# Kernel tuning notes

Hardware: AMD Instinct MI355X
Metric: run time of the kernel (lower is better)

## Reference

```python
import jax, jax.numpy as jnp
import numpy as np

N = 50000   # nodes
E = 800000  # edges (avg degree 16)
D = 96      # input feature dim
U = 96      # units (== D, so no dense_i projection)


def _glorot(key, fan_in, fan_out):
    limit = np.sqrt(6.0 / (fan_in + fan_out)).astype(np.float32)
    return jax.random.uniform(key, (fan_in, fan_out), jnp.float32, -limit, limit)


def setup_inputs() -> dict:
    key = jax.random.key(0)
    ks = jax.random.split(key, 8)
    X = jax.random.normal(ks[0], (N, D), jnp.float32)
    row = jax.random.randint(ks[1], (E,), 0, N, jnp.int32)   # destination nodes
    col = jax.random.randint(ks[2], (E,), 0, N, jnp.int32)   # source nodes
    a_vals = jax.random.uniform(ks[3], (E,), jnp.float32)    # adjacency values
    return {
        "X": X,
        "a_vals": a_vals,
        "Wn": _glorot(ks[4], D, U), "bn": jnp.zeros((U,), jnp.float32),
        "Wgi": _glorot(ks[5], D, U), "bgi": jnp.zeros((U,), jnp.float32),
        "Wgn": _glorot(ks[6], U, U), "bgn": jnp.zeros((U,), jnp.float32),
        "row": row, "col": col,
    }


def reference(X, a_vals, Wn, bn, Wgi, bgi, Wgn, bgn, row, col):
    # new_X = dense_n(X); new_X = A @ new_X  (SpMM via gather + segment_sum)
    newX = X @ Wn + bn                       # [N, U]
    msgs = a_vals[:, None] * newX[col]       # [E, U]
    agg = jax.ops.segment_sum(msgs, row, num_segments=N)  # [N, U]
    # gate = sigmoid(dense_gate_i(X) + dense_gate_n(agg))
    gate = jax.nn.sigmoid(X @ Wgi + bgi + agg @ Wgn + bgn)
    # units == inp_dim -> no dense_i; gated residual combine
    return agg * gate + X * (1.0 - gate)
```

## Files before the change

kernel.cpp:

```cpp
#include <hip/hip_runtime.h>
#include <math.h>


#define DU 96
#define DU4 24
#define CAP 64

typedef unsigned int uint;
typedef unsigned short ushort;
typedef __attribute__((ext_vector_type(8))) short short8;
typedef __attribute__((ext_vector_type(4))) float f32x4;

__device__ inline uint bf16r(float x) {
  uint u = __float_as_uint(x);
  return (u + 0x7FFFu + ((u >> 16) & 1u)) >> 16;
}

__global__ __launch_bounds__(256) void k_fuse1(
    const float* __restrict__ X, const float* __restrict__ Wn,
    const float* __restrict__ bn, const float* __restrict__ Wgi,
    const float* __restrict__ Wgn, const int* __restrict__ row,
    const int* __restrict__ col, const float* __restrict__ a_vals,
    ushort* __restrict__ Xb, ushort* __restrict__ newXb,
    ushort* __restrict__ WTgi, ushort* __restrict__ WTgn,
    int* __restrict__ cnt, int2* __restrict__ epad, int N, int E, int ntile) {
  __shared__ ushort WL[9216];
  __shared__ ushort Xs[64][104];
  const int tid = threadIdx.x;
  const int lane = tid & 63, w = tid >> 6;
  const int m = lane & 15, q = lane >> 4;

  if ((int)blockIdx.x < ntile) {
    if (blockIdx.x == 0) {
      for (int i = tid; i < DU * DU; i += 256) {
        int n = i / DU, k = i % DU;
        WTgi[i] = (ushort)bf16r(Wgi[k * DU + n]);
      }
    } else if (blockIdx.x == 1) {
      for (int i = tid; i < DU * DU; i += 256) {
        int n = i / DU, k = i % DU;
        WTgn[i] = (ushort)bf16r(Wgn[k * DU + n]);
      }
    }
    for (int idx = tid; idx < 9216; idx += 256) {
      int j = idx & 7, ln = (idx >> 3) & 63, tk = idx >> 9;
      int ks = tk / 6, t = tk % 6;
      int k = ks * 32 + (ln >> 4) * 8 + j;
      int n = t * 16 + (ln & 15);
      WL[idx] = (ushort)bf16r(Wn[k * DU + n]);
    }
    const int row0 = blockIdx.x * 64;
    for (int i = tid; i < 64 * 48; i += 256) {
      int r = i / 48, cu = i % 48;
      int gr = row0 + r;
      uint packed = 0;
      if (gr < N) {
        float2 v = ((const float2*)X)[(size_t)gr * 48 + cu];
        packed = bf16r(v.x) | (bf16r(v.y) << 16);
        ((uint*)Xb)[(size_t)gr * 48 + cu] = packed;
      }
      *(uint*)&Xs[r][cu * 2] = packed;
    }
    __syncthreads();

    f32x4 acc[6];
#pragma unroll
    for (int t = 0; t < 6; ++t) acc[t] = (f32x4){0.f, 0.f, 0.f, 0.f};
#pragma unroll
    for (int ks = 0; ks < 3; ++ks) {
      short8 af = *(const short8*)&Xs[w * 16 + m][ks * 32 + q * 8];
#pragma unroll
      for (int t = 0; t < 6; ++t) {
        short8 bf = *(const short8*)&WL[((ks * 6 + t) * 64 + lane) * 8];
        acc[t] = __builtin_amdgcn_mfma_f32_16x16x32_bf16(af, bf, acc[t], 0, 0, 0);
      }
    }
    __syncthreads();
#pragma unroll
    for (int t = 0; t < 6; ++t) {
      int c = t * 16 + m;
      float bb = bn[c];
#pragma unroll
      for (int i = 0; i < 4; ++i)
        Xs[w * 16 + q * 4 + i][c] = (ushort)bf16r(acc[t][i] + bb);
    }
    __syncthreads();
    for (int i = tid; i < 64 * 48; i += 256) {
      int r = i / 48, cu = i % 48;
      int gr = row0 + r;
      if (gr < N) ((uint*)newXb)[(size_t)gr * 48 + cu] = *(uint*)&Xs[r][cu * 2];
    }
  }

  {
    const int g = blockIdx.x & 7;
    const int sub = blockIdx.x >> 3;
    const int nsub = gridDim.x >> 3;
    const int d0 = (int)((long long)N * g >> 3);
    const int d1 = (int)((long long)N * (g + 1) >> 3);
    for (int i = sub * 256 + tid; i < E; i += nsub * 256) {
      int d = row[i];
      if (d >= d0 && d < d1) {
        int slot = atomicAdd(&cnt[d], 1);
        epad[(size_t)d * CAP + slot] = make_int2(col[i], __float_as_int(a_vals[i]));
      }
    }
  }
}

__global__ __launch_bounds__(256) void k_agg(const ushort* __restrict__ newXb,
                                             const int* __restrict__ cnt,
                                             const int2* __restrict__ epad,
                                             ushort* __restrict__ aggb, int N) {
  int i = blockIdx.x * 256 + threadIdx.x;
  int r = i / 12;
  int c = i % 12;
  if (r >= N) return;
  int e1 = cnt[r];
  if (e1 > CAP) e1 = CAP;
  const int2* ep = epad + (size_t)r * CAP;
  float accA[8], accB[8];
#pragma unroll
  for (int k = 0; k < 8; ++k) { accA[k] = 0.f; accB[k] = 0.f; }
  int e = 0;
  for (; e + 4 <= e1; e += 4) {
    int2 p0 = ep[e + 0];
    int2 p1 = ep[e + 1];
    int2 p2 = ep[e + 2];
    int2 p3 = ep[e + 3];
    uint4 v0 = *(const uint4*)(newXb + (size_t)p0.x * DU + c * 8);
    uint4 v1 = *(const uint4*)(newXb + (size_t)p1.x * DU + c * 8);
    uint4 v2 = *(const uint4*)(newXb + (size_t)p2.x * DU + c * 8);
    uint4 v3 = *(const uint4*)(newXb + (size_t)p3.x * DU + c * 8);
    float a0 = __int_as_float(p0.y), a1 = __int_as_float(p1.y);
    float a2 = __int_as_float(p2.y), a3 = __int_as_float(p3.y);
    accA[0] = fmaf(a0, __uint_as_float(v0.x << 16), accA[0]);
    accA[1] = fmaf(a0, __uint_as_float(v0.x & 0xFFFF0000u), accA[1]);
    accA[2] = fmaf(a0, __uint_as_float(v0.y << 16), accA[2]);
    accA[3] = fmaf(a0, __uint_as_float(v0.y & 0xFFFF0000u), accA[3]);
    accA[4] = fmaf(a0, __uint_as_float(v0.z << 16), accA[4]);
    accA[5] = fmaf(a0, __uint_as_float(v0.z & 0xFFFF0000u), accA[5]);
    accA[6] = fmaf(a0, __uint_as_float(v0.w << 16), accA[6]);
    accA[7] = fmaf(a0, __uint_as_float(v0.w & 0xFFFF0000u), accA[7]);
    accB[0] = fmaf(a1, __uint_as_float(v1.x << 16), accB[0]);
    accB[1] = fmaf(a1, __uint_as_float(v1.x & 0xFFFF0000u), accB[1]);
    accB[2] = fmaf(a1, __uint_as_float(v1.y << 16), accB[2]);
    accB[3] = fmaf(a1, __uint_as_float(v1.y & 0xFFFF0000u), accB[3]);
    accB[4] = fmaf(a1, __uint_as_float(v1.z << 16), accB[4]);
    accB[5] = fmaf(a1, __uint_as_float(v1.z & 0xFFFF0000u), accB[5]);
    accB[6] = fmaf(a1, __uint_as_float(v1.w << 16), accB[6]);
    accB[7] = fmaf(a1, __uint_as_float(v1.w & 0xFFFF0000u), accB[7]);
    accA[0] = fmaf(a2, __uint_as_float(v2.x << 16), accA[0]);
    accA[1] = fmaf(a2, __uint_as_float(v2.x & 0xFFFF0000u), accA[1]);
    accA[2] = fmaf(a2, __uint_as_float(v2.y << 16), accA[2]);
    accA[3] = fmaf(a2, __uint_as_float(v2.y & 0xFFFF0000u), accA[3]);
    accA[4] = fmaf(a2, __uint_as_float(v2.z << 16), accA[4]);
    accA[5] = fmaf(a2, __uint_as_float(v2.z & 0xFFFF0000u), accA[5]);
    accA[6] = fmaf(a2, __uint_as_float(v2.w << 16), accA[6]);
    accA[7] = fmaf(a2, __uint_as_float(v2.w & 0xFFFF0000u), accA[7]);
    accB[0] = fmaf(a3, __uint_as_float(v3.x << 16), accB[0]);
    accB[1] = fmaf(a3, __uint_as_float(v3.x & 0xFFFF0000u), accB[1]);
    accB[2] = fmaf(a3, __uint_as_float(v3.y << 16), accB[2]);
    accB[3] = fmaf(a3, __uint_as_float(v3.y & 0xFFFF0000u), accB[3]);
    accB[4] = fmaf(a3, __uint_as_float(v3.z << 16), accB[4]);
    accB[5] = fmaf(a3, __uint_as_float(v3.z & 0xFFFF0000u), accB[5]);
    accB[6] = fmaf(a3, __uint_as_float(v3.w << 16), accB[6]);
    accB[7] = fmaf(a3, __uint_as_float(v3.w & 0xFFFF0000u), accB[7]);
  }
  for (; e < e1; ++e) {
    int2 p = ep[e];
    uint4 v = *(const uint4*)(newXb + (size_t)p.x * DU + c * 8);
    float a = __int_as_float(p.y);
    accA[0] = fmaf(a, __uint_as_float(v.x << 16), accA[0]);
    accA[1] = fmaf(a, __uint_as_float(v.x & 0xFFFF0000u), accA[1]);
    accA[2] = fmaf(a, __uint_as_float(v.y << 16), accA[2]);
    accA[3] = fmaf(a, __uint_as_float(v.y & 0xFFFF0000u), accA[3]);
    accA[4] = fmaf(a, __uint_as_float(v.z << 16), accA[4]);
    accA[5] = fmaf(a, __uint_as_float(v.z & 0xFFFF0000u), accA[5]);
    accA[6] = fmaf(a, __uint_as_float(v.w << 16), accA[6]);
    accA[7] = fmaf(a, __uint_as_float(v.w & 0xFFFF0000u), accA[7]);
  }
#pragma unroll
  for (int k = 0; k < 8; ++k) accA[k] += accB[k];
  uint4 o;
  o.x = bf16r(accA[0]) | (bf16r(accA[1]) << 16);
  o.y = bf16r(accA[2]) | (bf16r(accA[3]) << 16);
  o.z = bf16r(accA[4]) | (bf16r(accA[5]) << 16);
  o.w = bf16r(accA[6]) | (bf16r(accA[7]) << 16);
  *(uint4*)(aggb + (size_t)r * DU + c * 8) = o;
}

__global__ __launch_bounds__(256) void k_gateM(const ushort* __restrict__ Xb,
                                               const ushort* __restrict__ aggb,
                                               const ushort* __restrict__ WTgi,
                                               const ushort* __restrict__ WTgn,
                                               const float* __restrict__ bgi,
                                               const float* __restrict__ bgn,
                                               const float* __restrict__ X,
                                               float* __restrict__ Out, int N) {
  __shared__ float Gs[64][100];
  const int tid = threadIdx.x;
  const int lane = tid & 63, w = tid >> 6;
  const int m = lane & 15, q = lane >> 4;
  const int row0 = blockIdx.x * 64;
  int ar = row0 + w * 16 + m;
  if (ar > N - 1) ar = N - 1;

  f32x4 acc[6];
#pragma unroll
  for (int t = 0; t < 6; ++t) acc[t] = (f32x4){0.f, 0.f, 0.f, 0.f};

#pragma unroll
  for (int ks = 0; ks < 3; ++ks) {
    short8 af = *(const short8*)(Xb + (size_t)ar * DU + ks * 32 + q * 8);
#pragma unroll
    for (int t = 0; t < 6; ++t) {
      short8 bf = *(const short8*)(WTgi + (size_t)(t * 16 + m) * DU + ks * 32 + q * 8);
      acc[t] = __builtin_amdgcn_mfma_f32_16x16x32_bf16(af, bf, acc[t], 0, 0, 0);
    }
  }
#pragma unroll
  for (int ks = 0; ks < 3; ++ks) {
    short8 af = *(const short8*)(aggb + (size_t)ar * DU + ks * 32 + q * 8);
#pragma unroll
    for (int t = 0; t < 6; ++t) {
      short8 bf = *(const short8*)(WTgn + (size_t)(t * 16 + m) * DU + ks * 32 + q * 8);
      acc[t] = __builtin_amdgcn_mfma_f32_16x16x32_bf16(af, bf, acc[t], 0, 0, 0);
    }
  }

#pragma unroll
  for (int t = 0; t < 6; ++t) {
    int c = t * 16 + m;
    float bb = bgi[c] + bgn[c];
#pragma unroll
    for (int i = 0; i < 4; ++i) {
      float z = acc[t][i] + bb;
      Gs[w * 16 + q * 4 + i][c] = 1.f / (1.f + __expf(-z));
    }
  }
  __syncthreads();

  for (int j = tid; j < 64 * DU4; j += 256) {
    int r = j / DU4, c = j % DU4;
    int gr = row0 + r;
    if (gr < N) {
      float4 xv = ((const float4*)X)[(size_t)gr * DU4 + c];
      uint2 av = ((const uint2*)aggb)[(size_t)gr * DU4 + c];
      float a0 = __uint_as_float(av.x << 16);
      float a1 = __uint_as_float(av.x & 0xFFFF0000u);
      float a2 = __uint_as_float(av.y << 16);
      float a3 = __uint_as_float(av.y & 0xFFFF0000u);
      const float* gp = &Gs[r][c * 4];
      float4 o;
      o.x = xv.x + gp[0] * (a0 - xv.x);
      o.y = xv.y + gp[1] * (a1 - xv.y);
      o.z = xv.z + gp[2] * (a2 - xv.z);
      o.w = xv.w + gp[3] * (a3 - xv.w);
      ((float4*)Out)[(size_t)gr * DU4 + c] = o;
    }
  }
}

extern "C" void kernel_launch(void* const* d_in, const int* in_sizes, int n_in,
                              void* d_out, int out_size, void* d_ws, size_t ws_size,
                              hipStream_t stream) {
  const float* X      = (const float*)d_in[0];
  const float* a_vals = (const float*)d_in[1];
  const float* Wn     = (const float*)d_in[2];
  const float* bn     = (const float*)d_in[3];
  const float* Wgi    = (const float*)d_in[4];
  const float* bgi    = (const float*)d_in[5];
  const float* Wgn    = (const float*)d_in[6];
  const float* bgn    = (const float*)d_in[7];
  const int*   row    = (const int*)d_in[8];
  const int*   col    = (const int*)d_in[9];
  float* out = (float*)d_out;

  const int N = in_sizes[0] / DU;
  const int E = in_sizes[1];
  const int ntile = (N + 63) / 64;
  const int G1 = ((ntile + 7) / 8) * 8;

  int2*   epad  = (int2*)d_ws;
  ushort* Xb    = (ushort*)(epad + (size_t)N * CAP + CAP);
  ushort* newXb = Xb + (size_t)N * DU;
  ushort* aggb  = newXb + (size_t)N * DU;
  ushort* WTgi  = aggb + (size_t)N * DU;
  ushort* WTgn  = WTgi + DU * DU;
  int*    cnt   = (int*)(WTgn + DU * DU);

  hipMemsetAsync(cnt, 0, (size_t)N * sizeof(int), stream);

  k_fuse1<<<G1, 256, 0, stream>>>(X, Wn, bn, Wgi, Wgn, row, col, a_vals,
                                  Xb, newXb, WTgi, WTgn, cnt, epad, N, E, ntile);
  k_agg  <<<((size_t)N * 12 + 255) / 256, 256, 0, stream>>>(newXb, cnt, epad, aggb, N);
  k_gateM<<<ntile, 256, 0, stream>>>(Xb, aggb, WTgi, WTgn, bgi, bgn, X, out, N);
}
```

Measured before the change: 187.5 us.

## Fuse SpMM aggregation into gate kernel via shared-memory agg tile

Merges the aggregation kernel into the gate/combine kernel. Each 512-thread block aggregates its 64 rows into shared memory and feeds that tile directly to the MFMA gate GEMM and the residual combine. This removes the aggb global round trip and one launch. It also switches the Xb/newXb writes in the first kernel to nontemporal stores. In exchange, the gather phase now has fewer threads in flight per row tile (768 work items per 512 threads), and the gate GEMM is split across 8 waves with 3 tiles each.

```diff
diff --git a/kernel.cpp b/kernel.cpp
--- a/kernel.cpp
+++ b/kernel.cpp
@@ -57,7 +57,7 @@
       if (gr < N) {
         float2 v = ((const float2*)X)[(size_t)gr * 48 + cu];
         packed = bf16r(v.x) | (bf16r(v.y) << 16);
-        ((uint*)Xb)[(size_t)gr * 48 + cu] = packed;
+        __builtin_nontemporal_store(packed, &((uint*)Xb)[(size_t)gr * 48 + cu]);
       }
       *(uint*)&Xs[r][cu * 2] = packed;
     }
@@ -88,7 +88,9 @@
     for (int i = tid; i < 64 * 48; i += 256) {
       int r = i / 48, cu = i % 48;
       int gr = row0 + r;
-      if (gr < N) ((uint*)newXb)[(size_t)gr * 48 + cu] = *(uint*)&Xs[r][cu * 2];
+      if (gr < N)
+        __builtin_nontemporal_store(*(uint*)&Xs[r][cu * 2],
+                                    &((uint*)newXb)[(size_t)gr * 48 + cu]);
     }
   }
 
@@ -108,145 +110,150 @@
   }
 }
 
-__global__ __launch_bounds__(256) void k_agg(const ushort* __restrict__ newXb,
-                                             const int* __restrict__ cnt,
-                                             const int2* __restrict__ epad,
-                                             ushort* __restrict__ aggb, int N) {
-  int i = blockIdx.x * 256 + threadIdx.x;
-  int r = i / 12;
-  int c = i % 12;
-  if (r >= N) return;
-  int e1 = cnt[r];
-  if (e1 > CAP) e1 = CAP;
-  const int2* ep = epad + (size_t)r * CAP;
-  float accA[8], accB[8];
-#pragma unroll
-  for (int k = 0; k < 8; ++k) { accA[k] = 0.f; accB[k] = 0.f; }
-  int e = 0;
-  for (; e + 4 <= e1; e += 4) {
-    int2 p0 = ep[e + 0];
-    int2 p1 = ep[e + 1];
-    int2 p2 = ep[e + 2];
-    int2 p3 = ep[e + 3];
-    uint4 v0 = *(const uint4*)(newXb + (size_t)p0.x * DU + c * 8);
-    uint4 v1 = *(const uint4*)(newXb + (size_t)p1.x * DU + c * 8);
-    uint4 v2 = *(const uint4*)(newXb + (size_t)p2.x * DU + c * 8);
-    uint4 v3 = *(const uint4*)(newXb + (size_t)p3.x * DU + c * 8);
-    float a0 = __int_as_float(p0.y), a1 = __int_as_float(p1.y);
-    float a2 = __int_as_float(p2.y), a3 = __int_as_float(p3.y);
-    accA[0] = fmaf(a0, __uint_as_float(v0.x << 16), accA[0]);
-    accA[1] = fmaf(a0, __uint_as_float(v0.x & 0xFFFF0000u), accA[1]);
-    accA[2] = fmaf(a0, __uint_as_float(v0.y << 16), accA[2]);
-    accA[3] = fmaf(a0, __uint_as_float(v0.y & 0xFFFF0000u), accA[3]);
-    accA[4] = fmaf(a0, __uint_as_float(v0.z << 16), accA[4]);
-    accA[5] = fmaf(a0, __uint_as_float(v0.z & 0xFFFF0000u), accA[5]);
-    accA[6] = fmaf(a0, __uint_as_float(v0.w << 16), accA[6]);
-    accA[7] = fmaf(a0, __uint_as_float(v0.w & 0xFFFF0000u), accA[7]);
-    accB[0] = fmaf(a1, __uint_as_float(v1.x << 16), accB[0]);
-    accB[1] = fmaf(a1, __uint_as_float(v1.x & 0xFFFF0000u), accB[1]);
-    accB[2] = fmaf(a1, __uint_as_float(v1.y << 16), accB[2]);
-    accB[3] = fmaf(a1, __uint_as_float(v1.y & 0xFFFF0000u), accB[3]);
-    accB[4] = fmaf(a1, __uint_as_float(v1.z << 16), accB[4]);
-    accB[5] = fmaf(a1, __uint_as_float(v1.z & 0xFFFF0000u), accB[5]);
-    accB[6] = fmaf(a1, __uint_as_float(v1.w << 16), accB[6]);
-    accB[7] = fmaf(a1, __uint_as_float(v1.w & 0xFFFF0000u), accB[7]);
-    accA[0] = fmaf(a2, __uint_as_float(v2.x << 16), accA[0]);
-    accA[1] = fmaf(a2, __uint_as_float(v2.x & 0xFFFF0000u), accA[1]);
-    accA[2] = fmaf(a2, __uint_as_float(v2.y << 16), accA[2]);
-    accA[3] = fmaf(a2, __uint_as_float(v2.y & 0xFFFF0000u), accA[3]);
-    accA[4] = fmaf(a2, __uint_as_float(v2.z << 16), accA[4]);
-    accA[5] = fmaf(a2, __uint_as_float(v2.z & 0xFFFF0000u), accA[5]);
-    accA[6] = fmaf(a2, __uint_as_float(v2.w << 16), accA[6]);
-    accA[7] = fmaf(a2, __uint_as_float(v2.w & 0xFFFF0000u), accA[7]);
-    accB[0] = fmaf(a3, __uint_as_float(v3.x << 16), accB[0]);
-    accB[1] = fmaf(a3, __uint_as_float(v3.x & 0xFFFF0000u), accB[1]);
-    accB[2] = fmaf(a3, __uint_as_float(v3.y << 16), accB[2]);
-    accB[3] = fmaf(a3, __uint_as_float(v3.y & 0xFFFF0000u), accB[3]);
-    accB[4] = fmaf(a3, __uint_as_float(v3.z << 16), accB[4]);
-    accB[5] = fmaf(a3, __uint_as_float(v3.z & 0xFFFF0000u), accB[5]);
-    accB[6] = fmaf(a3, __uint_as_float(v3.w << 16), accB[6]);
-    accB[7] = fmaf(a3, __uint_as_float(v3.w & 0xFFFF0000u), accB[7]);
-  }
-  for (; e < e1; ++e) {
-    int2 p = ep[e];
-    uint4 v = *(const uint4*)(newXb + (size_t)p.x * DU + c * 8);
-    float a = __int_as_float(p.y);
-    accA[0] = fmaf(a, __uint_as_float(v.x << 16), accA[0]);
-    accA[1] = fmaf(a, __uint_as_float(v.x & 0xFFFF0000u), accA[1]);
-    accA[2] = fmaf(a, __uint_as_float(v.y << 16), accA[2]);
-    accA[3] = fmaf(a, __uint_as_float(v.y & 0xFFFF0000u), accA[3]);
-    accA[4] = fmaf(a, __uint_as_float(v.z << 16), accA[4]);
-    accA[5] = fmaf(a, __uint_as_float(v.z & 0xFFFF0000u), accA[5]);
-    accA[6] = fmaf(a, __uint_as_float(v.w << 16), accA[6]);
-    accA[7] = fmaf(a, __uint_as_float(v.w & 0xFFFF0000u), accA[7]);
-  }
-#pragma unroll
-  for (int k = 0; k < 8; ++k) accA[k] += accB[k];
-  uint4 o;
-  o.x = bf16r(accA[0]) | (bf16r(accA[1]) << 16);
-  o.y = bf16r(accA[2]) | (bf16r(accA[3]) << 16);
-  o.z = bf16r(accA[4]) | (bf16r(accA[5]) << 16);
-  o.w = bf16r(accA[6]) | (bf16r(accA[7]) << 16);
-  *(uint4*)(aggb + (size_t)r * DU + c * 8) = o;
-}
-
-__global__ __launch_bounds__(256) void k_gateM(const ushort* __restrict__ Xb,
-                                               const ushort* __restrict__ aggb,
-                                               const ushort* __restrict__ WTgi,
-                                               const ushort* __restrict__ WTgn,
-                                               const float* __restrict__ bgi,
-                                               const float* __restrict__ bgn,
-                                               const float* __restrict__ X,
-                                               float* __restrict__ Out, int N) {
+__global__ __launch_bounds__(512) void k_aggGate(
+    const ushort* __restrict__ Xb, const ushort* __restrict__ newXb,
+    const int* __restrict__ cnt, const int2* __restrict__ epad,
+    const ushort* __restrict__ WTgi, const ushort* __restrict__ WTgn,
+    const float* __restrict__ bgi, const float* __restrict__ bgn,
+    const float* __restrict__ X, float* __restrict__ Out, int N) {
+  __shared__ ushort As[64][104];
   __shared__ float Gs[64][100];
   const int tid = threadIdx.x;
-  const int lane = tid & 63, w = tid >> 6;
+  const int lane = tid & 63;
   const int m = lane & 15, q = lane >> 4;
   const int row0 = blockIdx.x * 64;
-  int ar = row0 + w * 16 + m;
-  if (ar > N - 1) ar = N - 1;
-
-  f32x4 acc[6];
-#pragma unroll
-  for (int t = 0; t < 6; ++t) acc[t] = (f32x4){0.f, 0.f, 0.f, 0.f};
-
-#pragma unroll
-  for (int ks = 0; ks < 3; ++ks) {
-    short8 af = *(const short8*)(Xb + (size_t)ar * DU + ks * 32 + q * 8);
-#pragma unroll
-    for (int t = 0; t < 6; ++t) {
-      short8 bf = *(const short8*)(WTgi + (size_t)(t * 16 + m) * DU + ks * 32 + q * 8);
-      acc[t] = __builtin_amdgcn_mfma_f32_16x16x32_bf16(af, bf, acc[t], 0, 0, 0);
-    }
-  }
-#pragma unroll
-  for (int ks = 0; ks < 3; ++ks) {
-    short8 af = *(const short8*)(aggb + (size_t)ar * DU + ks * 32 + q * 8);
-#pragma unroll
-    for (int t = 0; t < 6; ++t) {
-      short8 bf = *(const short8*)(WTgn + (size_t)(t * 16 + m) * DU + ks * 32 + q * 8);
-      acc[t] = __builtin_amdgcn_mfma_f32_16x16x32_bf16(af, bf, acc[t], 0, 0, 0);
-    }
-  }
-
-#pragma unroll
-  for (int t = 0; t < 6; ++t) {
-    int c = t * 16 + m;
-    float bb = bgi[c] + bgn[c];
-#pragma unroll
-    for (int i = 0; i < 4; ++i) {
-      float z = acc[t][i] + bb;
-      Gs[w * 16 + q * 4 + i][c] = 1.f / (1.f + __expf(-z));
-    }
+
+  for (int j = tid; j < 64 * 12; j += 512) {
+    int lr = j / 12, c = j % 12;
+    int r = row0 + lr;
+    float accA[8], accB[8];
+#pragma unroll
+    for (int k = 0; k < 8; ++k) { accA[k] = 0.f; accB[k] = 0.f; }
+    if (r < N) {
+      int e1 = cnt[r];
+      if (e1 > CAP) e1 = CAP;
+      const int2* ep = epad + (size_t)r * CAP;
+      int e = 0;
+      for (; e + 4 <= e1; e += 4) {
+        int2 p0 = ep[e + 0];
+        int2 p1 = ep[e + 1];
+        int2 p2 = ep[e + 2];
+        int2 p3 = ep[e + 3];
+        uint4 v0 = *(const uint4*)(newXb + (size_t)p0.x * DU + c * 8);
+        uint4 v1 = *(const uint4*)(newXb + (size_t)p1.x * DU + c * 8);
+        uint4 v2 = *(const uint4*)(newXb + (size_t)p2.x * DU + c * 8);
+        uint4 v3 = *(const uint4*)(newXb + (size_t)p3.x * DU + c * 8);
+        float a0 = __int_as_float(p0.y), a1 = __int_as_float(p1.y);
+        float a2 = __int_as_float(p2.y), a3 = __int_as_float(p3.y);
+        accA[0] = fmaf(a0, __uint_as_float(v0.x << 16), accA[0]);
+        accA[1] = fmaf(a0, __uint_as_float(v0.x & 0xFFFF0000u), accA[1]);
+        accA[2] = fmaf(a0, __uint_as_float(v0.y << 16), accA[2]);
+        accA[3] = fmaf(a0, __uint_as_float(v0.y & 0xFFFF0000u), accA[3]);
+        accA[4] = fmaf(a0, __uint_as_float(v0.z << 16), accA[4]);
+        accA[5] = fmaf(a0, __uint_as_float(v0.z & 0xFFFF0000u), accA[5]);
+        accA[6] = fmaf(a0, __uint_as_float(v0.w << 16), accA[6]);
+        accA[7] = fmaf(a0, __uint_as_float(v0.w & 0xFFFF0000u), accA[7]);
+        accB[0] = fmaf(a1, __uint_as_float(v1.x << 16), accB[0]);
+        accB[1] = fmaf(a1, __uint_as_float(v1.x & 0xFFFF0000u), accB[1]);
+        accB[2] = fmaf(a1, __uint_as_float(v1.y << 16), accB[2]);
+        accB[3] = fmaf(a1, __uint_as_float(v1.y & 0xFFFF0000u), accB[3]);
+        accB[4] = fmaf(a1, __uint_as_float(v1.z << 16), accB[4]);
+        accB[5] = fmaf(a1, __uint_as_float(v1.z & 0xFFFF0000u), accB[5]);
+        accB[6] = fmaf(a1, __uint_as_float(v1.w << 16), accB[6]);
+        accB[7] = fmaf(a1, __uint_as_float(v1.w & 0xFFFF0000u), accB[7]);
+        accA[0] = fmaf(a2, __uint_as_float(v2.x << 16), accA[0]);
+        accA[1] = fmaf(a2, __uint_as_float(v2.x & 0xFFFF0000u), accA[1]);
+        accA[2] = fmaf(a2, __uint_as_float(v2.y << 16), accA[2]);
+        accA[3] = fmaf(a2, __uint_as_float(v2.y & 0xFFFF0000u), accA[3]);
+        accA[4] = fmaf(a2, __uint_as_float(v2.z << 16), accA[4]);
+        accA[5] = fmaf(a2, __uint_as_float(v2.z & 0xFFFF0000u), accA[5]);
+        accA[6] = fmaf(a2, __uint_as_float(v2.w << 16), accA[6]);
+        accA[7] = fmaf(a2, __uint_as_float(v2.w & 0xFFFF0000u), accA[7]);
+        accB[0] = fmaf(a3, __uint_as_float(v3.x << 16), accB[0]);
+        accB[1] = fmaf(a3, __uint_as_float(v3.x & 0xFFFF0000u), accB[1]);
+        accB[2] = fmaf(a3, __uint_as_float(v3.y << 16), accB[2]);
+        accB[3] = fmaf(a3, __uint_as_float(v3.y & 0xFFFF0000u), accB[3]);
+        accB[4] = fmaf(a3, __uint_as_float(v3.z << 16), accB[4]);
+        accB[5] = fmaf(a3, __uint_as_float(v3.z & 0xFFFF0000u), accB[5]);
+        accB[6] = fmaf(a3, __uint_as_float(v3.w << 16), accB[6]);
+        accB[7] = fmaf(a3, __uint_as_float(v3.w & 0xFFFF0000u), accB[7]);
+      }
+      for (; e < e1; ++e) {
+        int2 p = ep[e];
+        uint4 v = *(const uint4*)(newXb + (size_t)p.x * DU + c * 8);
+        float a = __int_as_float(p.y);
+        accA[0] = fmaf(a, __uint_as_float(v.x << 16), accA[0]);
+        accA[1] = fmaf(a, __uint_as_float(v.x & 0xFFFF0000u), accA[1]);
+        accA[2] = fmaf(a, __uint_as_float(v.y << 16), accA[2]);
+        accA[3] = fmaf(a, __uint_as_float(v.y & 0xFFFF0000u), accA[3]);
+        accA[4] = fmaf(a, __uint_as_float(v.z << 16), accA[4]);
+        accA[5] = fmaf(a, __uint_as_float(v.z & 0xFFFF0000u), accA[5]);
+        accA[6] = fmaf(a, __uint_as_float(v.w << 16), accA[6]);
+        accA[7] = fmaf(a, __uint_as_float(v.w & 0xFFFF0000u), accA[7]);
+      }
+#pragma unroll
+      for (int k = 0; k < 8; ++k) accA[k] += accB[k];
+    }
+    uint4 o;
+    o.x = bf16r(accA[0]) | (bf16r(accA[1]) << 16);
+    o.y = bf16r(accA[2]) | (bf16r(accA[3]) << 16);
+    o.z = bf16r(accA[4]) | (bf16r(accA[5]) << 16);
+    o.w = bf16r(accA[6]) | (bf16r(accA[7]) << 16);
+    *(uint4*)&As[lr][c * 8] = o;
   }
   __syncthreads();
 
-  for (int j = tid; j < 64 * DU4; j += 256) {
+  {
+    const int wv = tid >> 6;
+    const int rg = wv >> 1;
+    const int ch = wv & 1;
+    int ar = row0 + rg * 16 + m;
+    if (ar > N - 1) ar = N - 1;
+    const int lr = rg * 16 + m;
+
+    f32x4 acc[3];
+#pragma unroll
+    for (int t = 0; t < 3; ++t) acc[t] = (f32x4){0.f, 0.f, 0.f, 0.f};
+
+#pragma unroll
+    for (int ks = 0; ks < 3; ++ks) {
+      short8 af = *(const short8*)(Xb + (size_t)ar * DU + ks * 32 + q * 8);
+#pragma unroll
+      for (int tt = 0; tt < 3; ++tt) {
+        int t = ch * 3 + tt;
+        short8 bf = *(const short8*)(WTgi + (size_t)(t * 16 + m) * DU + ks * 32 + q * 8);
+        acc[tt] = __builtin_amdgcn_mfma_f32_16x16x32_bf16(af, bf, acc[tt], 0, 0, 0);
+      }
+    }
+#pragma unroll
+    for (int ks = 0; ks < 3; ++ks) {
+      short8 af = *(const short8*)&As[lr][ks * 32 + q * 8];
+#pragma unroll
+      for (int tt = 0; tt < 3; ++tt) {
+        int t = ch * 3 + tt;
+        short8 bf = *(const short8*)(WTgn + (size_t)(t * 16 + m) * DU + ks * 32 + q * 8);
+        acc[tt] = __builtin_amdgcn_mfma_f32_16x16x32_bf16(af, bf, acc[tt], 0, 0, 0);
+      }
+    }
+#pragma unroll
+    for (int tt = 0; tt < 3; ++tt) {
+      int c = (ch * 3 + tt) * 16 + m;
+      float bb = bgi[c] + bgn[c];
+#pragma unroll
+      for (int i = 0; i < 4; ++i) {
+        float z = acc[tt][i] + bb;
+        Gs[rg * 16 + q * 4 + i][c] = 1.f / (1.f + __expf(-z));
+      }
+    }
+  }
+  __syncthreads();
+
+  for (int j = tid; j < 64 * DU4; j += 512) {
     int r = j / DU4, c = j % DU4;
     int gr = row0 + r;
     if (gr < N) {
       float4 xv = ((const float4*)X)[(size_t)gr * DU4 + c];
-      uint2 av = ((const uint2*)aggb)[(size_t)gr * DU4 + c];
+      uint2 av = *(const uint2*)&As[r][c * 4];
       float a0 = __uint_as_float(av.x << 16);
       float a1 = __uint_as_float(av.x & 0xFFFF0000u);
       float a2 = __uint_as_float(av.y << 16);
@@ -285,8 +292,7 @@
   int2*   epad  = (int2*)d_ws;
   ushort* Xb    = (ushort*)(epad + (size_t)N * CAP + CAP);
   ushort* newXb = Xb + (size_t)N * DU;
-  ushort* aggb  = newXb + (size_t)N * DU;
-  ushort* WTgi  = aggb + (size_t)N * DU;
+  ushort* WTgi  = newXb + (size_t)N * DU;
   ushort* WTgn  = WTgi + DU * DU;
   int*    cnt   = (int*)(WTgn + DU * DU);
 
@@ -294,6 +300,6 @@
 
   k_fuse1<<<G1, 256, 0, stream>>>(X, Wn, bn, Wgi, Wgn, row, col, a_vals,
                                   Xb, newXb, WTgi, WTgn, cnt, epad, N, E, ntile);
-  k_agg  <<<((size_t)N * 12 + 255) / 256, 256, 0, stream>>>(newXb, cnt, epad, aggb, N);
-  k_gateM<<<ntile, 256, 0, stream>>>(Xb, aggb, WTgi, WTgn, bgi, bgn, X, out, N);
+  k_aggGate<<<ntile, 512, 0, stream>>>(Xb, newXb, cnt, epad, WTgi, WTgn,
+                                       bgi, bgn, X, out, N);
 }
```

Result: no change. 187.6 us (+0.1%).
